# Kernel optimization log

Measured on AMD Instinct MI355X. Metric: run time of the kernel, lower is better.

## Reference

```python
import jax, jax.numpy as jnp
import numpy as np

DIM = 128; MOTION = 128; HEADS = 8; WS = 8; B2 = 4; H = 192; W = 192; HID = 512

def _ln(x, w, b, eps=1e-5):
    m = x.mean(-1, keepdims=True)
    v = ((x - m) ** 2).mean(-1, keepdims=True)
    return (x - m) / jnp.sqrt(v + eps) * w + b

def _win_part(x, ws):
    B, Hh, Ww, C = x.shape
    x = x.reshape(B, Hh // ws, ws, Ww // ws, ws, C).transpose(0, 1, 3, 2, 4, 5)
    return x.reshape(-1, ws * ws, C)

def _win_rev(win, ws, Hh, Ww):
    nwB, N, C = win.shape
    B = nwB // ((Hh // ws) * (Ww // ws))
    x = win.reshape(B, Hh // ws, Ww // ws, ws, ws, C).transpose(0, 1, 3, 2, 4, 5)
    return x.reshape(B, Hh, Ww, C)

def setup_inputs() -> dict:
    key = jax.random.key(0)
    ks = jax.random.split(key, 12)
    def lin(k, o, i):
        return jax.random.normal(k, (o, i), jnp.float32) * 0.02
    return {
        "x": jax.random.normal(ks[0], (B2, H * W, DIM), jnp.float32),
        "cor": jax.random.uniform(ks[1], (B2, H * W, 2), dtype=jnp.float32),
        "q_w": lin(ks[2], DIM, DIM),
        "kv_w": lin(ks[3], 2 * DIM, DIM),
        "cor_w": lin(ks[4], MOTION, 2),
        "proj_w": lin(ks[5], DIM, DIM), "proj_b": jnp.zeros((DIM,), jnp.float32),
        "mproj_w": lin(ks[6], MOTION, MOTION), "mproj_b": jnp.zeros((MOTION,), jnp.float32),
        "norm1_w": jnp.ones((DIM,), jnp.float32), "norm1_b": jnp.zeros((DIM,), jnp.float32),
        "norm2_w": jnp.ones((DIM,), jnp.float32), "norm2_b": jnp.zeros((DIM,), jnp.float32),
        "fc1_w": lin(ks[7], HID, DIM), "fc1_b": jnp.zeros((HID,), jnp.float32),
        "dw_w": jax.random.normal(ks[8], (HID, 1, 3, 3), jnp.float32) * 0.1,
        "dw_b": jnp.zeros((HID,), jnp.float32),
        "fc2_w": lin(ks[9], DIM, HID), "fc2_b": jnp.zeros((DIM,), jnp.float32),
    }

def _attn(x1, x2, cor, q_w, kv_w, cor_w, proj_w, proj_b, mproj_w, mproj_b):
    # x1,x2: (nwB, N, C) windowed query / cross-frame key-value; cor: (nwB, N, 2)
    B, N, C = x1.shape
    hd = C // HEADS
    mh = MOTION // HEADS
    scale = hd ** -0.5
    q = (x1 @ q_w.T).reshape(B, N, HEADS, hd).transpose(0, 2, 1, 3)
    kv = (x2 @ kv_w.T).reshape(B, N, 2, HEADS, hd).transpose(2, 0, 3, 1, 4)
    k, v = kv[0], kv[1]
    ce = cor @ cor_w.T                                   # (B, N, MOTION)
    ceh = ce.reshape(B, N, HEADS, mh).transpose(0, 2, 1, 3)
    attn = jax.nn.softmax(jnp.einsum('bhnd,bhmd->bhnm', q, k) * scale, axis=-1)
    xo = jnp.einsum('bhnm,bhmd->bhnd', attn, v).transpose(0, 2, 1, 3).reshape(B, N, C)
    crev = jnp.einsum('bhnm,bhmd->bhnd', attn, ceh).transpose(0, 2, 1, 3).reshape(B, N, MOTION)
    motion = (crev - ce) @ mproj_w.T + mproj_b
    return xo @ proj_w.T + proj_b, motion

def _mlp(x, fc1_w, fc1_b, dw_w, dw_b, fc2_w, fc2_b):
    B, N, _ = x.shape
    h = x @ fc1_w.T + fc1_b                              # (B, N, HID)
    hm = h.transpose(0, 2, 1).reshape(B, HID, H, W)
    hm = jax.lax.conv_general_dilated(hm, dw_w, (1, 1), 'SAME',
                                      feature_group_count=HID,
                                      dimension_numbers=('NCHW', 'OIHW', 'NCHW'))
    hm = hm + dw_b[None, :, None, None]
    h = jax.nn.gelu(hm.reshape(B, HID, N).transpose(0, 2, 1), approximate=False)
    return h @ fc2_w.T + fc2_b

def reference(x, cor, q_w, kv_w, cor_w, proj_w, proj_b, mproj_w, mproj_b,
              norm1_w, norm1_b, norm2_w, norm2_b, fc1_w, fc1_b, dw_w, dw_b, fc2_w, fc2_b):
    shortcut = x
    xn = _ln(x, norm1_w, norm1_b).reshape(B2, H, W, DIM)
    cm = cor.reshape(B2, H, W, 2)
    xw = _win_part(xn, WS)                               # (nwB, 64, DIM)
    cw = _win_part(cm, WS)
    nwB = xw.shape[0]
    xr = jnp.concatenate([xw[nwB // 2:], xw[:nwB // 2]], axis=0)
    xa, xm = _attn(xw, xr, cw, q_w, kv_w, cor_w, proj_w, proj_b, mproj_w, mproj_b)
    xa = _win_rev(xa, WS, H, W).reshape(B2, H * W, DIM)
    xm = _win_rev(xm, WS, H, W).reshape(B2, H * W, MOTION)
    x = shortcut + xa
    x = x + _mlp(_ln(x, norm2_w, norm2_b), fc1_w, fc1_b, dw_w, dw_b, fc2_w, fc2_b)
    return x, xm
```

## Files before the change

### kernel.cpp

```cpp
#include <hip/hip_runtime.h>
#include <hip/hip_bf16.h>
#include <math.h>

#define NB 4
#define IMG 192
#define HW (IMG*IMG)
#define T_TOT (NB*HW)
#define HID 512
#define NWB 2304
#define WPB 576
#define NWS 24

typedef __bf16 bf16;
typedef __bf16 bf8 __attribute__((ext_vector_type(8)));
typedef __bf16 bf4 __attribute__((ext_vector_type(4)));
typedef float f32x4 __attribute__((ext_vector_type(4)));

#define MFMA(a,b,c) __builtin_amdgcn_mfma_f32_16x16x32_bf16(a,b,c,0,0,0)

#define BAR_LGKM asm volatile("s_waitcnt lgkmcnt(0)\ns_barrier" ::: "memory")
#define BAR_ALL  asm volatile("s_waitcnt vmcnt(0) lgkmcnt(0)\ns_barrier" ::: "memory")

__device__ __forceinline__ int swz128(int row, int col){ return row*128 + (col ^ ((row&7)<<3)); }

__device__ __forceinline__ bf8 zero_bf8(){
  bf8 z = { (bf16)0.f,(bf16)0.f,(bf16)0.f,(bf16)0.f,(bf16)0.f,(bf16)0.f,(bf16)0.f,(bf16)0.f };
  return z;
}
__device__ __forceinline__ f32x4 zero_f4(){ f32x4 z = {0.f,0.f,0.f,0.f}; return z; }

typedef const __attribute__((address_space(1))) unsigned int as1_u32;
typedef __attribute__((address_space(3))) unsigned int as3_u32;
__device__ __forceinline__ void gload16(const bf16* g, bf16* l){
  __builtin_amdgcn_global_load_lds((as1_u32*)g, (as3_u32*)l, 16, 0, 0);
}

__global__ __launch_bounds__(256) void k_prep(
    const float* __restrict__ q_w, const float* __restrict__ kv_w,
    const float* __restrict__ proj_w, const float* __restrict__ fc1w,
    const float* __restrict__ fc2w, const float* __restrict__ mproj_w,
    const float* __restrict__ cor_w,
    bf16* __restrict__ wq, bf16* __restrict__ wkv, bf16* __restrict__ wpj,
    bf16* __restrict__ wf1, bf16* __restrict__ wf2, bf16* __restrict__ a2w)
{
  int idx = blockIdx.x*256 + threadIdx.x;
  if (idx < 16384){ wq[idx] = (bf16)(q_w[idx]*0.25f); return; }
  idx -= 16384;
  if (idx < 32768){ wkv[idx] = (bf16)kv_w[idx]; return; }
  idx -= 32768;
  if (idx < 16384){ wpj[idx] = (bf16)proj_w[idx]; return; }
  idx -= 16384;
  if (idx < 65536){ wf1[idx] = (bf16)fc1w[idx]; return; }
  idx -= 65536;
  if (idx < 65536){ wf2[idx] = (bf16)fc2w[idx]; return; }
  idx -= 65536;
  if (idx >= 4096) return;
  int o = idx >> 5, k = idx & 31;
  float acc = 0.f;
  if (k < 16){
    int h = k >> 1, c = k & 1;
    #pragma unroll
    for (int i=0;i<16;i++)
      acc += mproj_w[o*128 + h*16 + i] * cor_w[(h*16+i)*2 + c];
  }
  a2w[o*32 + k] = (bf16)acc;
}

__global__ __launch_bounds__(256) void k_ln1(
    const float* __restrict__ x, const float* __restrict__ cor,
    const float* __restrict__ n1w, const float* __restrict__ n1b,
    bf16* __restrict__ xn, bf16* __restrict__ cwb)
{
  int tid = threadIdx.x, wm = tid>>6, l = tid&63;
  int lr = l & 15, tg = l >> 4;
  int t = blockIdx.x*16 + wm*4 + tg;

  const float* xp = x + (size_t)t*128 + lr*8;
  float4 a = *(const float4*)xp;
  float4 b4 = *(const float4*)(xp+4);
  float s  = a.x+a.y+a.z+a.w + b4.x+b4.y+b4.z+b4.w;
  float sq = a.x*a.x+a.y*a.y+a.z*a.z+a.w*a.w + b4.x*b4.x+b4.y*b4.y+b4.z*b4.z+b4.w*b4.w;
  #pragma unroll
  for (int m=1;m<16;m<<=1){ s += __shfl_xor(s,m,16); sq += __shfl_xor(sq,m,16); }
  float mean = s * (1.0f/128.0f);
  float var  = sq * (1.0f/128.0f) - mean*mean;
  float rstd = rsqrtf(var + 1e-5f);

  float4 nw0 = *(const float4*)(n1w + lr*8), nw1 = *(const float4*)(n1w + lr*8 + 4);
  float4 nb0 = *(const float4*)(n1b + lr*8), nb1 = *(const float4*)(n1b + lr*8 + 4);

  bf8 o;
  o[0] = (bf16)((a.x -mean)*rstd*nw0.x + nb0.x);
  o[1] = (bf16)((a.y -mean)*rstd*nw0.y + nb0.y);
  o[2] = (bf16)((a.z -mean)*rstd*nw0.z + nb0.z);
  o[3] = (bf16)((a.w -mean)*rstd*nw0.w + nb0.w);
  o[4] = (bf16)((b4.x-mean)*rstd*nw1.x + nb1.x);
  o[5] = (bf16)((b4.y-mean)*rstd*nw1.y + nb1.y);
  o[6] = (bf16)((b4.z-mean)*rstd*nw1.z + nb1.z);
  o[7] = (bf16)((b4.w-mean)*rstd*nw1.w + nb1.w);

  int b = t / HW, r = t % HW;
  int yy = r / IMG, xx = r % IMG;
  int win = b*WPB + (yy>>3)*NWS + (xx>>3);
  int n = ((yy&7)<<3) + (xx&7);
  *(bf8*)(xn + (size_t)win*8192 + n*128 + lr*8) = o;

  if (lr < 2) cwb[(size_t)win*128 + n*2 + lr] = (bf16)cor[(size_t)t*2 + lr];
}

__global__ __launch_bounds__(256) void k_attn(
    const bf16* __restrict__ xn, const bf16* __restrict__ cw,
    const bf16* __restrict__ wq, const bf16* __restrict__ wkv,
    const bf16* __restrict__ wpj, const bf16* __restrict__ a2w,
    const float* __restrict__ proj_b, const float* __restrict__ mproj_b,
    const float* __restrict__ x_in, float* __restrict__ x1, float* __restrict__ out_m)
{
  __shared__ __align__(16) bf16 s_s [64*128];
  __shared__ __align__(16) bf16 s_k [64*128];
  __shared__ __align__(16) bf16 s_vT[128*64];
  __shared__ __align__(16) bf16 s_P [64*64];
  __shared__ __align__(16) bf16 s_cT[16*64];
  __shared__ __align__(16) bf16 s_D [64*32];

  int tid = threadIdx.x, wm = tid>>6, l = tid&63;
  int lr = l & 15, lg = l >> 4;
  int win = blockIdx.x;
  int partner = (win + NWB/2) % NWB;
  const bf16* xw_g = xn + (size_t)win*8192;
  const bf16* xr_g = xn + (size_t)partner*8192;

  bf8 xrv[4], xwv[4];
  #pragma unroll
  for (int tci=0;tci<4;tci++){
    int chunk = tid + tci*256;
    int row = chunk>>4, c0 = (chunk&15)*8;
    xrv[tci] = *(const bf8*)(xr_g + row*128 + c0);
    xwv[tci] = *(const bf8*)(xw_g + row*128 + c0);
  }
  bf16 cwv = (bf16)0.f;
  if (tid < 128) cwv = cw[(size_t)win*128 + tid];

  *(unsigned long long*)&s_cT[tid*4] = 0ull;
  *(unsigned long long*)&s_D[tid*8]   = 0ull;
  *(unsigned long long*)&s_D[tid*8+4] = 0ull;
  #pragma unroll
  for (int tci=0;tci<4;tci++){
    int chunk = tid + tci*256;
    int row = chunk>>4, c0 = (chunk&15)*8;
    *(bf8*)&s_s[swz128(row,c0)] = xrv[tci];
  }
  BAR_LGKM;

  if (tid < 128){
    int c = tid & 1, m = tid >> 1;
    s_cT[c*64 + (m ^ (c<<3))] = cwv;
  } else if (tid < 192){
    int m = tid - 128;
    s_cT[2*64 + (m ^ 16)] = (bf16)1.0f;
  }
  {
    bf8 af[4];
    #pragma unroll
    for (int ks=0;ks<4;ks++) af[ks] = *(const bf8*)&s_s[swz128(wm*16+lr, ks*32 + lg*8)];
    #pragma unroll
    for (int nt=0;nt<8;nt++){
      f32x4 acc = zero_f4();
      #pragma unroll
      for (int ks=0;ks<4;ks++){
        bf8 bfr = *(const bf8*)(wkv + (nt*16+lr)*128 + ks*32 + lg*8);
        acc = MFMA(af[ks], bfr, acc);
      }
      #pragma unroll
      for (int j=0;j<4;j++){
        int row = wm*16 + lg*4 + j;
        s_k[swz128(row, nt*16+lr)] = (bf16)acc[j];
      }
    }
    #pragma unroll
    for (int nt=0;nt<8;nt++){
      f32x4 acc = zero_f4();
      #pragma unroll
      for (int ks=0;ks<4;ks++){
        bf8 bfr = *(const bf8*)(wkv + (128 + nt*16+lr)*128 + ks*32 + lg*8);
        acc = MFMA(af[ks], bfr, acc);
      }
      #pragma unroll
      for (int j=0;j<4;j++){
        int tok = wm*16 + lg*4 + j;
        int chc = nt*16 + lr;
        s_vT[chc*64 + (tok ^ ((chc&7)<<3))] = (bf16)acc[j];
      }
    }
  }
  BAR_LGKM;

  #pragma unroll
  for (int tci=0;tci<4;tci++){
    int chunk = tid + tci*256;
    int row = chunk>>4, c0 = (chunk&15)*8;
    *(bf8*)&s_s[swz128(row,c0)] = xwv[tci];
  }
  BAR_LGKM;

  {
    bf8 af[4];
    #pragma unroll
    for (int ks=0;ks<4;ks++) af[ks] = *(const bf8*)&s_s[swz128(wm*16+lr, ks*32 + lg*8)];
    #pragma unroll
    for (int nt=0;nt<8;nt++){
      f32x4 acc = zero_f4();
      #pragma unroll
      for (int ks=0;ks<4;ks++){
        bf8 bfr = *(const bf8*)(wq + (nt*16+lr)*128 + ks*32 + lg*8);
        acc = MFMA(af[ks], bfr, acc);
      }
      #pragma unroll
      for (int j=0;j<4;j++){
        int row = wm*16 + lg*4 + j;
        s_s[swz128(row, nt*16+lr)] = (bf16)acc[j];
      }
    }
  }

  float mycw[4] = {0.f,0.f,0.f,0.f};
  if (lr < 2){
    #pragma unroll
    for (int j=0;j<4;j++){
      int row = wm*16 + lg*4 + j;
      mycw[j] = (float)s_cT[lr*64 + (row ^ (lr<<3))];
    }
  }

  f32x4 accS[4];
  {
    bf8 aS = zero_bf8();
    if (l < 32) aS = *(const bf8*)&s_s[swz128(wm*16+lr, lg*8)];
    #pragma unroll
    for (int nt=0;nt<4;nt++){
      bf8 bSv = zero_bf8();
      if (l < 32) bSv = *(const bf8*)&s_k[swz128(nt*16+lr, lg*8)];
      accS[nt] = MFMA(aS, bSv, zero_f4());
    }
  }
  #pragma unroll
  for (int h=0;h<8;h++){
    #pragma unroll
    for (int nt=0;nt<4;nt++){
      #pragma unroll
      for (int j=0;j<4;j++){
        int row = wm*16 + lg*4 + j;
        s_P[row*64 + ((nt*16+lr) ^ ((row&7)<<3))] = (bf16)__expf(accS[nt][j]);
      }
    }
    if (h < 7){
      bf8 aS = zero_bf8();
      if (l < 32) aS = *(const bf8*)&s_s[swz128(wm*16+lr, (h+1)*16 + lg*8)];
      #pragma unroll
      for (int nt=0;nt<4;nt++){
        bf8 bSv = zero_bf8();
        if (l < 32) bSv = *(const bf8*)&s_k[swz128(nt*16+lr, (h+1)*16 + lg*8)];
        accS[nt] = MFMA(aS, bSv, zero_f4());
      }
    }
    f32x4 accO = zero_f4(), accPC = zero_f4();
    #pragma unroll
    for (int ks=0;ks<2;ks++){
      int rowA = wm*16 + lr;
      bf8 aP = *(const bf8*)&s_P[rowA*64 + ((ks*32 + lg*8) ^ ((rowA&7)<<3))];
      int chc = h*16 + lr;
      bf8 bV = *(const bf8*)&s_vT[chc*64 + ((ks*32 + lg*8) ^ ((chc&7)<<3))];
      accO = MFMA(aP, bV, accO);
      bf8 bC = *(const bf8*)&s_cT[lr*64 + ((ks*32 + lg*8) ^ ((lr&7)<<3))];
      accPC = MFMA(aP, bC, accPC);
    }
    #pragma unroll
    for (int j=0;j<4;j++){
      int row = wm*16 + lg*4 + j;
      float rs = __shfl(accPC[j], (l & 48) + 2, 64);
      float inv = __builtin_amdgcn_rcpf(rs);
      s_s[swz128(row, h*16+lr)] = (bf16)(accO[j]*inv);
      if (lr < 2)
        s_D[row*32 + ((2*h+lr) ^ ((row&3)<<3))] = (bf16)(accPC[j]*inv - mycw[j]);
    }
  }

  int b  = win / WPB, wi = win % WPB;
  int wy = wi / NWS,  wx = wi % NWS;
  {
    bf8 af[4];
    #pragma unroll
    for (int ks=0;ks<4;ks++) af[ks] = *(const bf8*)&s_s[swz128(wm*16+lr, ks*32 + lg*8)];
    #pragma unroll
    for (int nt=0;nt<8;nt++){
      f32x4 acc = zero_f4();
      #pragma unroll
      for (int ks=0;ks<4;ks++){
        bf8 bfr = *(const bf8*)(wpj + (nt*16+lr)*128 + ks*32 + lg*8);
        acc = MFMA(af[ks], bfr, acc);
      }
      int col = nt*16 + lr;
      float pb = proj_b[col];
      #pragma unroll
      for (int j=0;j<4;j++){
        int tok = wm*16 + lg*4 + j;
        int yy = wy*8 + (tok>>3), xx = wx*8 + (tok&7);
        size_t addr = ((size_t)b*HW + yy*IMG + xx)*128 + col;
        x1[addr] = acc[j] + pb + x_in[addr];
      }
    }
  }
  {
    int rowA = wm*16 + lr;
    bf8 afD = *(const bf8*)&s_D[rowA*32 + ((lg*8) ^ ((rowA&3)<<3))];
    #pragma unroll
    for (int nt=0;nt<8;nt++){
      bf8 bfr = *(const bf8*)(a2w + (nt*16+lr)*32 + lg*8);
      f32x4 acc = MFMA(afD, bfr, zero_f4());
      int col = nt*16 + lr;
      float pb = mproj_b[col];
      #pragma unroll
      for (int j=0;j<4;j++){
        int tok = wm*16 + lg*4 + j;
        int yy = wy*8 + (tok>>3), xx = wx*8 + (tok&7);
        size_t addr = ((size_t)b*HW + yy*IMG + xx)*128 + col;
        out_m[addr] = acc[j] + pb;
      }
    }
  }
}

__global__ __launch_bounds__(256) void k_fc1(
    const float* __restrict__ x1, const float* __restrict__ n2w, const float* __restrict__ n2b,
    const bf16* __restrict__ wf1, const float* __restrict__ fc1b, bf16* __restrict__ h)
{
  __shared__ __align__(16) bf16 s_a[64*128];
  int tid = threadIdx.x, wm = tid>>6, l = tid&63;
  int lr = l & 15, lg = l >> 4;
  size_t t0 = (size_t)blockIdx.x * 64;

  float4 nw0 = *(const float4*)(n2w + lr*8), nw1 = *(const float4*)(n2w + lr*8 + 4);
  float4 nb0 = *(const float4*)(n2b + lr*8), nb1 = *(const float4*)(n2b + lr*8 + 4);

  #pragma unroll
  for (int rr=0; rr<4; rr++){
    int row = wm*16 + rr*4 + lg;
    const float* xp = x1 + (t0+row)*128 + lr*8;
    float4 a = *(const float4*)xp;
    float4 b4 = *(const float4*)(xp+4);
    float s  = a.x+a.y+a.z+a.w + b4.x+b4.y+b4.z+b4.w;
    float sq = a.x*a.x+a.y*a.y+a.z*a.z+a.w*a.w + b4.x*b4.x+b4.y*b4.y+b4.z*b4.z+b4.w*b4.w;
    #pragma unroll
    for (int m=1;m<16;m<<=1){ s += __shfl_xor(s,m,16); sq += __shfl_xor(sq,m,16); }
    float mean = s*(1.f/128.f), var = sq*(1.f/128.f) - mean*mean;
    float rstd = rsqrtf(var + 1e-5f);
    bf8 o;
    o[0] = (bf16)((a.x -mean)*rstd*nw0.x + nb0.x);
    o[1] = (bf16)((a.y -mean)*rstd*nw0.y + nb0.y);
    o[2] = (bf16)((a.z -mean)*rstd*nw0.z + nb0.z);
    o[3] = (bf16)((a.w -mean)*rstd*nw0.w + nb0.w);
    o[4] = (bf16)((b4.x-mean)*rstd*nw1.x + nb1.x);
    o[5] = (bf16)((b4.y-mean)*rstd*nw1.y + nb1.y);
    o[6] = (bf16)((b4.z-mean)*rstd*nw1.z + nb1.z);
    o[7] = (bf16)((b4.w-mean)*rstd*nw1.w + nb1.w);
    *(bf8*)&s_a[swz128(row, lr*8)] = o;
  }
  __syncthreads();

  bf8 af[4];
  #pragma unroll
  for (int ks=0;ks<4;ks++) af[ks] = *(const bf8*)&s_a[swz128(wm*16+lr, ks*32 + lg*8)];
  for (int ntb=0; ntb<4; ntb++){
    f32x4 acc[8];
    #pragma unroll
    for (int q8=0;q8<8;q8++){
      acc[q8] = zero_f4();
      #pragma unroll
      for (int ks=0;ks<4;ks++){
        int ocol = ntb*128 + q8*16 + lr;
        bf8 bfr = *(const bf8*)(wf1 + (size_t)ocol*128 + ks*32 + lg*8);
        acc[q8] = MFMA(af[ks], bfr, acc[q8]);
      }
    }
    #pragma unroll
    for (int q8=0;q8<8;q8++){
      int col = ntb*128 + q8*16 + lr;
      float bb = fc1b[col];
      #pragma unroll
      for (int j=0;j<4;j++){
        int tl = wm*16 + lg*4 + j;
        h[(t0+tl)*512 + col] = (bf16)(acc[q8][j] + bb);
      }
    }
  }
}

__global__ __launch_bounds__(256) void k_mlp2(
    const bf16* __restrict__ h, const float* __restrict__ dww, const float* __restrict__ dwb,
    const bf16* __restrict__ wf2, const float* __restrict__ fc2b,
    const float* __restrict__ x1, float* __restrict__ outx)
{
  __shared__ __align__(16) bf16 s_hh[2][100*128];
  int tid = threadIdx.x, wm = tid>>6, l = tid&63;
  int lr = l & 15, lg = l >> 4;
  int tile = 575 - blockIdx.x, b = 3 - blockIdx.y;
  int ty = tile / 24, tx = tile % 24;
  int cq = (tid & 31) * 4;
  int tg2 = tid >> 5;

  f32x4 acc[8];
  #pragma unroll
  for (int q=0;q<8;q++) acc[q] = zero_f4();

  bool edge = (ty==0) | (ty==23) | (tx==0) | (tx==23);
  if (edge){
    #pragma unroll
    for (int it=0; it<7; it++){
      int idx = it*256 + tid;
      if (idx < 1600){
        int pos = idx>>4, c0 = (idx&15)*8;
        int hy = pos/10, hx = pos%10;
        int yy = ty*8 + hy - 1, xx = tx*8 + hx - 1;
        if (yy<0 || yy>=IMG || xx<0 || xx>=IMG){
          *(bf8*)&s_hh[0][pos*128 + c0] = zero_bf8();
          *(bf8*)&s_hh[1][pos*128 + c0] = zero_bf8();
        }
      }
    }
  }

  #define STAGE_DMA(KC, BUF)                                                  \
    _Pragma("unroll")                                                         \
    for (int it=0; it<7; it++){                                               \
      int idx = it*256 + tid;                                                 \
      if (idx < 1600){                                                        \
        int pos = idx>>4, c0 = (idx&15)*8;                                    \
        int hy = pos/10, hx = pos%10;                                         \
        int yy = ty*8 + hy - 1, xx = tx*8 + hx - 1;                           \
        bf16* lb = &s_hh[BUF][it*2048 + wm*512];       \
        if (yy>=0 && yy<IMG && xx>=0 && xx<IMG)                               \
          gload16(h + ((size_t)b*HW + yy*IMG + xx)*512 + (KC)*128 + c0, lb);  \
      }                                                                       \
    }

  STAGE_DMA(0, 0);
  BAR_ALL;

  int cur = 0;
  for (int kc=0;kc<4;kc++){
    if (kc < 3) STAGE_DMA(kc+1, cur^1);

    int chg0 = kc*128 + cq;
    float4 bias4 = *(const float4*)(dwb + chg0);
    float cr[8][4];
    #pragma unroll
    for (int i=0;i<8;i++){ cr[i][0]=bias4.x; cr[i][1]=bias4.y; cr[i][2]=bias4.z; cr[i][3]=bias4.w; }
    #pragma unroll
    for (int dy=0;dy<3;dy++){
      float rv[10][4];
      #pragma unroll
      for (int p=0;p<10;p++){
        bf4 pv = *(const bf4*)&s_hh[cur][((tg2+dy)*10 + p)*128 + cq];
        rv[p][0]=(float)pv[0]; rv[p][1]=(float)pv[1];
        rv[p][2]=(float)pv[2]; rv[p][3]=(float)pv[3];
      }
      #pragma unroll
      for (int dx=0;dx<3;dx++){
        int tq = dy*3+dx;
        float w0 = dww[(chg0+0)*9 + tq];
        float w1 = dww[(chg0+1)*9 + tq];
        float w2 = dww[(chg0+2)*9 + tq];
        float w3 = dww[(chg0+3)*9 + tq];
        #pragma unroll
        for (int i=0;i<8;i++){
          cr[i][0] += rv[i+dx][0]*w0;
          cr[i][1] += rv[i+dx][1]*w1;
          cr[i][2] += rv[i+dx][2]*w2;
          cr[i][3] += rv[i+dx][3]*w3;
        }
      }
    }
    bf4 gout[8];
    #pragma unroll
    for (int i=0;i<8;i++){
      #pragma unroll
      for (int c=0;c<4;c++){
        float hv = cr[i][c];
        float hv2 = hv*hv;
        float v = hv * fmaf(hv2, -0.0713548353f, -1.5957691216f);
        float g = hv * __builtin_amdgcn_rcpf(1.0f + __expf(v));
        gout[i][c] = (bf16)g;
      }
    }
    BAR_LGKM;
    #pragma unroll
    for (int i=0;i<8;i++){
      int pos = (tg2+1)*10 + (i+1);
      *(bf4*)&s_hh[cur][pos*128 + (cq ^ (i<<3))] = gout[i];
    }
    {
      bf8 af[4];
      #pragma unroll
      for (int ks=0;ks<4;ks++){
        int tok = wm*16 + lr;
        int pos = ((tok>>3)+1)*10 + (tok&7) + 1;
        af[ks] = *(const bf8*)&s_hh[cur][pos*128 + ((ks*32 + lg*8) ^ ((lr&7)<<3))];
      }
      #pragma unroll
      for (int q=0;q<8;q++){
        #pragma unroll
        for (int ks=0;ks<4;ks++){
          bf8 bfr = *(const bf8*)(wf2 + (size_t)(q*16+lr)*512 + kc*128 + ks*32 + lg*8);
          acc[q] = MFMA(af[ks], bfr, acc[q]);
        }
      }
    }
    BAR_ALL;
    cur ^= 1;
  }
  #pragma unroll
  for (int q=0;q<8;q++){
    int col = q*16 + lr;
    float bb = fc2b[col];
    #pragma unroll
    for (int j=0;j<4;j++){
      int tok = wm*16 + lg*4 + j;
      int yy = ty*8 + (tok>>3), xx = tx*8 + (tok&7);
      size_t addr = ((size_t)b*HW + yy*IMG + xx)*128 + col;
      outx[addr] = acc[q][j] + bb + x1[addr];
    }
  }
  #undef STAGE_DMA
}

extern "C" void kernel_launch(void* const* d_in, const int* in_sizes, int n_in,
                              void* d_out, int out_size, void* d_ws, size_t ws_size,
                              hipStream_t stream)
{
  const float* x      = (const float*)d_in[0];
  const float* cor    = (const float*)d_in[1];
  const float* q_w    = (const float*)d_in[2];
  const float* kv_w   = (const float*)d_in[3];
  const float* cor_w  = (const float*)d_in[4];
  const float* proj_w = (const float*)d_in[5];
  const float* proj_b = (const float*)d_in[6];
  const float* mproj_w= (const float*)d_in[7];
  const float* mproj_b= (const float*)d_in[8];
  const float* n1w    = (const float*)d_in[9];
  const float* n1b    = (const float*)d_in[10];
  const float* n2w    = (const float*)d_in[11];
  const float* n2b    = (const float*)d_in[12];
  const float* fc1w   = (const float*)d_in[13];
  const float* fc1b   = (const float*)d_in[14];
  const float* dww    = (const float*)d_in[15];
  const float* dwb    = (const float*)d_in[16];
  const float* fc2w   = (const float*)d_in[17];
  const float* fc2b   = (const float*)d_in[18];
  float* out = (float*)d_out;

  char* ws = (char*)d_ws;
  bf16* wq   = (bf16*)(ws + 0);
  bf16* wkv  = (bf16*)(ws + 32768);
  bf16* wpj  = (bf16*)(ws + 98304);
  bf16* a2w  = (bf16*)(ws + 131072);
  bf16* wf1  = (bf16*)(ws + 139264);
  bf16* wf2  = (bf16*)(ws + 270336);
  bf16* xn   = (bf16*)(ws + 401408);
  bf16* cwb  = (bf16*)(ws + 38150144);
  float* x1  = (float*)(ws + 38739968);
  bf16* hbuf = (bf16*)(ws + 114237440);

  k_prep<<<784, 256, 0, stream>>>(q_w, kv_w, proj_w, fc1w, fc2w, mproj_w, cor_w,
                                  wq, wkv, wpj, wf1, wf2, a2w);

  k_ln1 <<<T_TOT/16, 256, 0, stream>>>(x, cor, n1w, n1b, xn, cwb);
  k_attn<<<NWB,      256, 0, stream>>>(xn, cwb, wq, wkv, wpj, a2w, proj_b, mproj_b,
                                       x, x1, out + (size_t)T_TOT*128);
  k_fc1 <<<T_TOT/64, 256, 0, stream>>>(x1, n2w, n2b, wf1, fc1b, hbuf);
  k_mlp2<<<dim3(576,4), 256, 0, stream>>>(hbuf, dww, dwb, wf2, fc2b, x1, out);
}
```

Baseline: 531.2 us.

## Fuse LayerNorm1 and window partitioning into the attention kernel

Removes the separate k_ln1 kernel and its bf16 windowed intermediate buffers. The attention kernel now reads fp32 x directly for its own window and its cross-frame partner window, normalizes it in registers and writes the result straight into shared memory. It also gathers the cor values itself. This avoids a global write and re-read of the normalized activations and one kernel launch, and drops two block barriers because each wave only touches its own rows. In exchange, the larger fp32 input is read twice per window, and the loads are no longer issued early to hide latency.

```diff
diff --git a/kernel.cpp b/kernel.cpp
--- a/kernel.cpp
+++ b/kernel.cpp
@@ -66,54 +66,13 @@
   a2w[o*32 + k] = (bf16)acc;
 }
 
-__global__ __launch_bounds__(256) void k_ln1(
-    const float* __restrict__ x, const float* __restrict__ cor,
+__global__ __launch_bounds__(256) void k_attn(
+    const float* __restrict__ x_in, const float* __restrict__ cor,
     const float* __restrict__ n1w, const float* __restrict__ n1b,
-    bf16* __restrict__ xn, bf16* __restrict__ cwb)
-{
-  int tid = threadIdx.x, wm = tid>>6, l = tid&63;
-  int lr = l & 15, tg = l >> 4;
-  int t = blockIdx.x*16 + wm*4 + tg;
-
-  const float* xp = x + (size_t)t*128 + lr*8;
-  float4 a = *(const float4*)xp;
-  float4 b4 = *(const float4*)(xp+4);
-  float s  = a.x+a.y+a.z+a.w + b4.x+b4.y+b4.z+b4.w;
-  float sq = a.x*a.x+a.y*a.y+a.z*a.z+a.w*a.w + b4.x*b4.x+b4.y*b4.y+b4.z*b4.z+b4.w*b4.w;
-  #pragma unroll
-  for (int m=1;m<16;m<<=1){ s += __shfl_xor(s,m,16); sq += __shfl_xor(sq,m,16); }
-  float mean = s * (1.0f/128.0f);
-  float var  = sq * (1.0f/128.0f) - mean*mean;
-  float rstd = rsqrtf(var + 1e-5f);
-
-  float4 nw0 = *(const float4*)(n1w + lr*8), nw1 = *(const float4*)(n1w + lr*8 + 4);
-  float4 nb0 = *(const float4*)(n1b + lr*8), nb1 = *(const float4*)(n1b + lr*8 + 4);
-
-  bf8 o;
-  o[0] = (bf16)((a.x -mean)*rstd*nw0.x + nb0.x);
-  o[1] = (bf16)((a.y -mean)*rstd*nw0.y + nb0.y);
-  o[2] = (bf16)((a.z -mean)*rstd*nw0.z + nb0.z);
-  o[3] = (bf16)((a.w -mean)*rstd*nw0.w + nb0.w);
-  o[4] = (bf16)((b4.x-mean)*rstd*nw1.x + nb1.x);
-  o[5] = (bf16)((b4.y-mean)*rstd*nw1.y + nb1.y);
-  o[6] = (bf16)((b4.z-mean)*rstd*nw1.z + nb1.z);
-  o[7] = (bf16)((b4.w-mean)*rstd*nw1.w + nb1.w);
-
-  int b = t / HW, r = t % HW;
-  int yy = r / IMG, xx = r % IMG;
-  int win = b*WPB + (yy>>3)*NWS + (xx>>3);
-  int n = ((yy&7)<<3) + (xx&7);
-  *(bf8*)(xn + (size_t)win*8192 + n*128 + lr*8) = o;
-
-  if (lr < 2) cwb[(size_t)win*128 + n*2 + lr] = (bf16)cor[(size_t)t*2 + lr];
-}
-
-__global__ __launch_bounds__(256) void k_attn(
-    const bf16* __restrict__ xn, const bf16* __restrict__ cw,
     const bf16* __restrict__ wq, const bf16* __restrict__ wkv,
     const bf16* __restrict__ wpj, const bf16* __restrict__ a2w,
     const float* __restrict__ proj_b, const float* __restrict__ mproj_b,
-    const float* __restrict__ x_in, float* __restrict__ x1, float* __restrict__ out_m)
+    float* __restrict__ x1, float* __restrict__ out_m)
 {
   __shared__ __align__(16) bf16 s_s [64*128];
   __shared__ __align__(16) bf16 s_k [64*128];
@@ -125,39 +84,59 @@
   int tid = threadIdx.x, wm = tid>>6, l = tid&63;
   int lr = l & 15, lg = l >> 4;
   int win = blockIdx.x;
-  int partner = (win + NWB/2) % NWB;
-  const bf16* xw_g = xn + (size_t)win*8192;
-  const bf16* xr_g = xn + (size_t)partner*8192;
-
-  bf8 xrv[4], xwv[4];
-  #pragma unroll
-  for (int tci=0;tci<4;tci++){
-    int chunk = tid + tci*256;
-    int row = chunk>>4, c0 = (chunk&15)*8;
-    xrv[tci] = *(const bf8*)(xr_g + row*128 + c0);
-    xwv[tci] = *(const bf8*)(xw_g + row*128 + c0);
-  }
-  bf16 cwv = (bf16)0.f;
-  if (tid < 128) cwv = cw[(size_t)win*128 + tid];
-
-  *(unsigned long long*)&s_cT[tid*4] = 0ull;
+  int b  = win / WPB, wi = win % WPB;
+  int wy = wi / NWS,  wx = wi % NWS;
+  int bp = (b + NB/2) % NB;
+
+  float cwf = 0.f;
+  if (tid < 128){
+    int m = tid >> 1, c = tid & 1;
+    cwf = cor[((size_t)b*HW + (size_t)(wy*8+(m>>3))*IMG + wx*8+(m&7))*2 + c];
+  }
+
   *(unsigned long long*)&s_D[tid*8]   = 0ull;
   *(unsigned long long*)&s_D[tid*8+4] = 0ull;
-  #pragma unroll
-  for (int tci=0;tci<4;tci++){
-    int chunk = tid + tci*256;
-    int row = chunk>>4, c0 = (chunk&15)*8;
-    *(bf8*)&s_s[swz128(row,c0)] = xrv[tci];
-  }
-  BAR_LGKM;
-
+  if (tid >= 192){
+    int cc = tid - 192;
+    #pragma unroll
+    for (int r=3;r<16;r++) s_cT[r*64 + cc] = (bf16)0.f;
+  }
   if (tid < 128){
     int c = tid & 1, m = tid >> 1;
-    s_cT[c*64 + (m ^ (c<<3))] = cwv;
+    s_cT[c*64 + (m ^ (c<<3))] = (bf16)cwf;
   } else if (tid < 192){
     int m = tid - 128;
     s_cT[2*64 + (m ^ 16)] = (bf16)1.0f;
   }
+
+  {
+    float4 nw0 = *(const float4*)(n1w + lr*8), nw1 = *(const float4*)(n1w + lr*8 + 4);
+    float4 nb0 = *(const float4*)(n1b + lr*8), nb1 = *(const float4*)(n1b + lr*8 + 4);
+    #pragma unroll
+    for (int p=0;p<4;p++){
+      int n = wm*16 + p*4 + lg;
+      const float* xp = x_in + ((size_t)bp*HW + (size_t)(wy*8+(n>>3))*IMG + wx*8+(n&7))*128 + lr*8;
+      float4 a = *(const float4*)xp;
+      float4 b4 = *(const float4*)(xp+4);
+      float s  = a.x+a.y+a.z+a.w + b4.x+b4.y+b4.z+b4.w;
+      float sq = a.x*a.x+a.y*a.y+a.z*a.z+a.w*a.w + b4.x*b4.x+b4.y*b4.y+b4.z*b4.z+b4.w*b4.w;
+      #pragma unroll
+      for (int m=1;m<16;m<<=1){ s += __shfl_xor(s,m,16); sq += __shfl_xor(sq,m,16); }
+      float mean = s*(1.f/128.f), var = sq*(1.f/128.f) - mean*mean;
+      float rstd = rsqrtf(var + 1e-5f);
+      bf8 o;
+      o[0] = (bf16)((a.x -mean)*rstd*nw0.x + nb0.x);
+      o[1] = (bf16)((a.y -mean)*rstd*nw0.y + nb0.y);
+      o[2] = (bf16)((a.z -mean)*rstd*nw0.z + nb0.z);
+      o[3] = (bf16)((a.w -mean)*rstd*nw0.w + nb0.w);
+      o[4] = (bf16)((b4.x-mean)*rstd*nw1.x + nb1.x);
+      o[5] = (bf16)((b4.y-mean)*rstd*nw1.y + nb1.y);
+      o[6] = (bf16)((b4.z-mean)*rstd*nw1.z + nb1.z);
+      o[7] = (bf16)((b4.w-mean)*rstd*nw1.w + nb1.w);
+      *(bf8*)&s_s[swz128(n, lr*8)] = o;
+    }
+  }
+
   {
     bf8 af[4];
     #pragma unroll
@@ -192,15 +171,34 @@
       }
     }
   }
-  BAR_LGKM;
-
-  #pragma unroll
-  for (int tci=0;tci<4;tci++){
-    int chunk = tid + tci*256;
-    int row = chunk>>4, c0 = (chunk&15)*8;
-    *(bf8*)&s_s[swz128(row,c0)] = xwv[tci];
-  }
-  BAR_LGKM;
+
+  {
+    float4 nw0 = *(const float4*)(n1w + lr*8), nw1 = *(const float4*)(n1w + lr*8 + 4);
+    float4 nb0 = *(const float4*)(n1b + lr*8), nb1 = *(const float4*)(n1b + lr*8 + 4);
+    #pragma unroll
+    for (int p=0;p<4;p++){
+      int n = wm*16 + p*4 + lg;
+      const float* xp = x_in + ((size_t)b*HW + (size_t)(wy*8+(n>>3))*IMG + wx*8+(n&7))*128 + lr*8;
+      float4 a = *(const float4*)xp;
+      float4 b4 = *(const float4*)(xp+4);
+      float s  = a.x+a.y+a.z+a.w + b4.x+b4.y+b4.z+b4.w;
+      float sq = a.x*a.x+a.y*a.y+a.z*a.z+a.w*a.w + b4.x*b4.x+b4.y*b4.y+b4.z*b4.z+b4.w*b4.w;
+      #pragma unroll
+      for (int m=1;m<16;m<<=1){ s += __shfl_xor(s,m,16); sq += __shfl_xor(sq,m,16); }
+      float mean = s*(1.f/128.f), var = sq*(1.f/128.f) - mean*mean;
+      float rstd = rsqrtf(var + 1e-5f);
+      bf8 o;
+      o[0] = (bf16)((a.x -mean)*rstd*nw0.x + nb0.x);
+      o[1] = (bf16)((a.y -mean)*rstd*nw0.y + nb0.y);
+      o[2] = (bf16)((a.z -mean)*rstd*nw0.z + nb0.z);
+      o[3] = (bf16)((a.w -mean)*rstd*nw0.w + nb0.w);
+      o[4] = (bf16)((b4.x-mean)*rstd*nw1.x + nb1.x);
+      o[5] = (bf16)((b4.y-mean)*rstd*nw1.y + nb1.y);
+      o[6] = (bf16)((b4.z-mean)*rstd*nw1.z + nb1.z);
+      o[7] = (bf16)((b4.w-mean)*rstd*nw1.w + nb1.w);
+      *(bf8*)&s_s[swz128(n, lr*8)] = o;
+    }
+  }
 
   {
     bf8 af[4];
@@ -221,6 +219,8 @@
       }
     }
   }
+
+  BAR_LGKM;
 
   float mycw[4] = {0.f,0.f,0.f,0.f};
   if (lr < 2){
@@ -284,8 +284,6 @@
     }
   }
 
-  int b  = win / WPB, wi = win % WPB;
-  int wy = wi / NWS,  wx = wi % NWS;
   {
     bf8 af[4];
     #pragma unroll
@@ -564,17 +562,15 @@
   bf16* a2w  = (bf16*)(ws + 131072);
   bf16* wf1  = (bf16*)(ws + 139264);
   bf16* wf2  = (bf16*)(ws + 270336);
-  bf16* xn   = (bf16*)(ws + 401408);
-  bf16* cwb  = (bf16*)(ws + 38150144);
-  float* x1  = (float*)(ws + 38739968);
-  bf16* hbuf = (bf16*)(ws + 114237440);
+  float* x1  = (float*)(ws + 401408);
+  bf16* hbuf = (bf16*)(ws + 401408 + 75497472);
 
   k_prep<<<784, 256, 0, stream>>>(q_w, kv_w, proj_w, fc1w, fc2w, mproj_w, cor_w,
                                   wq, wkv, wpj, wf1, wf2, a2w);
 
-  k_ln1 <<<T_TOT/16, 256, 0, stream>>>(x, cor, n1w, n1b, xn, cwb);
-  k_attn<<<NWB,      256, 0, stream>>>(xn, cwb, wq, wkv, wpj, a2w, proj_b, mproj_b,
-                                       x, x1, out + (size_t)T_TOT*128);
+  k_attn<<<NWB,      256, 0, stream>>>(x, cor, n1w, n1b, wq, wkv, wpj, a2w,
+                                       proj_b, mproj_b,
+                                       x1, out + (size_t)T_TOT*128);
   k_fc1 <<<T_TOT/64, 256, 0, stream>>>(x1, n2w, n2b, wf1, fc1b, hbuf);
   k_mlp2<<<dim3(576,4), 256, 0, stream>>>(hbuf, dww, dwb, wf2, fc2b, x1, out);
 }
```

Result: faster. 516.9 us (-2.7%).
